# Kernel optimization log

Measured on AMD Instinct MI355X. Metric: run time of the kernel, lower is better.

The kernel has to match this reference:

```python
import jax, jax.numpy as jnp
import numpy as np

B, N, C = 2, 2048, 768
H = 12
HD = C // H  # 64
EPS = 1e-6


def setup_inputs() -> dict:
    key = jax.random.key(0)
    ks = jax.random.split(key, 6)
    x = jax.random.normal(ks[0], (B, N, C), dtype=jnp.float32)
    # Xavier-uniform-ish init for kernels
    lim_qkv = float(np.sqrt(6.0 / (C + 3 * C)))
    lim_proj = float(np.sqrt(6.0 / (C + C)))
    qkv_kernel = jax.random.uniform(ks[1], (C, 3 * C), minval=-lim_qkv, maxval=lim_qkv, dtype=jnp.float32)
    qkv_bias = jnp.zeros((3 * C,), dtype=jnp.float32)
    proj_kernel = jax.random.uniform(ks[2], (C, C), minval=-lim_proj, maxval=lim_proj, dtype=jnp.float32)
    proj_bias = jnp.zeros((C,), dtype=jnp.float32)
    q_norm_w = jnp.ones((HD,), dtype=jnp.float32)
    k_norm_w = jnp.ones((HD,), dtype=jnp.float32)
    # Standard RoPE tables: freqs over half the head dim, tiled to full head_dim
    half = HD // 2
    inv_freq = 1.0 / (10000.0 ** (jnp.arange(0, half, dtype=jnp.float32) / half))
    t = jnp.arange(N, dtype=jnp.float32)
    freqs = jnp.outer(t, inv_freq)               # (N, HD/2)
    emb = jnp.concatenate([freqs, freqs], axis=-1)  # (N, HD)
    rope_cos = jnp.cos(emb)
    rope_sin = jnp.sin(emb)
    return {"x": x, "rope_cos": rope_cos, "rope_sin": rope_sin,
            "qkv_kernel": qkv_kernel, "qkv_bias": qkv_bias,
            "proj_kernel": proj_kernel, "proj_bias": proj_bias,
            "q_norm_w": q_norm_w, "k_norm_w": k_norm_w}


def _rms_norm(x, w):
    var = jnp.mean(x * x, axis=-1, keepdims=True)
    return x * jax.lax.rsqrt(var + EPS) * w


def _rope(x, cos, sin):
    # x: (B, H, N, HD); cos/sin: (N, HD)
    half = x.shape[-1] // 2
    x1, x2 = x[..., :half], x[..., half:]
    rot = jnp.concatenate([-x2, x1], axis=-1)
    return x * cos + rot * sin


def reference(x, rope_cos, rope_sin, qkv_kernel, qkv_bias, proj_kernel, proj_bias, q_norm_w, k_norm_w):
    b, n, c = x.shape
    qkv = x @ qkv_kernel + qkv_bias                       # (B, N, 3C)
    qkv = qkv.reshape(b, n, 3, H, HD).transpose(2, 0, 3, 1, 4)  # (3, B, H, N, HD)
    q, k, v = qkv[0], qkv[1], qkv[2]
    q = _rope(_rms_norm(q, q_norm_w), rope_cos, rope_sin)
    k = _rope(_rms_norm(k, k_norm_w), rope_cos, rope_sin)
    scale = 1.0 / jnp.sqrt(jnp.float32(HD)).astype(x.dtype)
    attn = jnp.einsum('bhqd,bhkd->bhqk', q, k) * scale    # (B, H, N, N)
    attn = jax.nn.softmax(attn, axis=-1)
    out = jnp.einsum('bhqk,bhkd->bhqd', attn, v)          # (B, H, N, HD)
    out = out.swapaxes(1, 2).reshape(b, n, c)
    return out @ proj_kernel + proj_bias
```

## Files before the change

### kernel.cpp

```cpp
#include <hip/hip_runtime.h>
#include <math.h>

#define B_    2
#define N_    2048
#define C_    768
#define H_    12
#define HD_   64
#define NROWS (B_*N_)
#define QKVC  (3*C_)
#define EPSV  1e-6f
#define SCALE 0.125f
#define LOG2E 1.44269504088896f
#define SMAX  12.0f

typedef unsigned short u16;
typedef short bf16x8 __attribute__((ext_vector_type(8)));
typedef float f32x4  __attribute__((ext_vector_type(4)));

__device__ __forceinline__ float b2f(u16 u) {
    unsigned v = ((unsigned)u) << 16;
    return __builtin_bit_cast(float, v);
}
__device__ __forceinline__ u16 f2b(float f) {
    unsigned u = __builtin_bit_cast(unsigned, f);
    u += 0x7fffu + ((u >> 16) & 1u);
    return (u16)(u >> 16);
}
__device__ __forceinline__ unsigned pk2(float a, float b) {
#if __has_builtin(__builtin_amdgcn_cvt_pk_bf16_f32)
    auto r = __builtin_amdgcn_cvt_pk_bf16_f32(a, b);
    return __builtin_bit_cast(unsigned, r);
#else
    return (unsigned)f2b(a) | ((unsigned)f2b(b) << 16);
#endif
}
__device__ __forceinline__ float fexp2(float x) {
#if __has_builtin(__builtin_amdgcn_exp2f)
    return __builtin_amdgcn_exp2f(x);
#else
    return exp2f(x);
#endif
}
__device__ __forceinline__ void gload_lds16(const void* g, void* l) {
    __builtin_amdgcn_global_load_lds(
        (const __attribute__((address_space(1))) unsigned int*)g,
        (__attribute__((address_space(3))) unsigned int*)l, 16, 0, 0);
}

__global__ __launch_bounds__(256)
void cvt_bf16_kernel(const float* __restrict__ src, u16* __restrict__ dst) {
    const int i = (blockIdx.x * 256 + threadIdx.x) * 4;
    const float4 v = *(const float4*)(src + i);
    uint2 o = { pk2(v.x, v.y), pk2(v.z, v.w) };
    *(uint2*)(dst + i) = o;
}

__global__ __launch_bounds__(256)
void wtrans_kernel(const float* __restrict__ W, u16* __restrict__ Wt,
                   int K, int N) {
    __shared__ float T[64][65];
    const int k0 = blockIdx.y * 64, n0 = blockIdx.x * 64;
    const int t = threadIdx.x, r = t >> 6, c = t & 63;
#pragma unroll
    for (int p = 0; p < 16; ++p) {
        const int kl = p * 4 + r;
        T[kl][c] = W[(size_t)(k0 + kl) * N + n0 + c];
    }
    __syncthreads();
#pragma unroll
    for (int p = 0; p < 16; ++p) {
        const int nl = p * 4 + r;
        Wt[(size_t)(n0 + nl) * K + k0 + c] = f2b(T[c][nl]);
    }
}

template <bool BF16OUT>
__global__ __launch_bounds__(256)
void gemm_tn_kernel(const u16* __restrict__ A, const u16* __restrict__ Bt,
                    const float* __restrict__ bias, void* __restrict__ Cout,
                    int M, int N, int K) {
    __shared__ __attribute__((aligned(16))) u16 As[128 * 32];
    __shared__ __attribute__((aligned(16))) u16 Bs[128 * 32];
    const int tid = threadIdx.x;
    const int w = tid >> 6, l = tid & 63;
    const int lq = l & 15, quad = l >> 4;
    const int mbase = blockIdx.y * 128, nbase = blockIdx.x * 128;

    f32x4 acc[4][4];
    const f32x4 z4 = {0.f, 0.f, 0.f, 0.f};
#pragma unroll
    for (int mb = 0; mb < 4; ++mb)
#pragma unroll
        for (int nb = 0; nb < 4; ++nb) acc[mb][nb] = z4;

    const int srow = (l >> 2);
    const int sdc  = (l & 3) ^ ((l >> 2) & 3);

    for (int k0 = 0; k0 < K; k0 += 32) {
#pragma unroll
        for (int cc = 0; cc < 2; ++cc) {
            const int c = 2 * w + cc;
            const int row = 16 * c + srow;
            gload_lds16(A  + (size_t)(mbase + row) * K + k0 + sdc * 8, &As[c * 512]);
            gload_lds16(Bt + (size_t)(nbase + row) * K + k0 + sdc * 8, &Bs[c * 512]);
        }
        __syncthreads();

        bf16x8 af[4], bfr[4];
#pragma unroll
        for (int mb = 0; mb < 4; ++mb)
            af[mb] = *(const bf16x8*)
                &As[((w >> 1) * 64 + mb * 16 + lq) * 32 + ((quad ^ (lq & 3)) * 8)];
#pragma unroll
        for (int nb = 0; nb < 4; ++nb)
            bfr[nb] = *(const bf16x8*)
                &Bs[((w & 1) * 64 + nb * 16 + lq) * 32 + ((quad ^ (lq & 3)) * 8)];
#pragma unroll
        for (int mb = 0; mb < 4; ++mb)
#pragma unroll
            for (int nb = 0; nb < 4; ++nb)
                acc[mb][nb] = __builtin_amdgcn_mfma_f32_16x16x32_bf16(
                    af[mb], bfr[nb], acc[mb][nb], 0, 0, 0);
        __syncthreads();
    }

#pragma unroll
    for (int nb = 0; nb < 4; ++nb) {
        const int col = nbase + (w & 1) * 64 + nb * 16 + lq;
        const float bv = bias[col];
#pragma unroll
        for (int mb = 0; mb < 4; ++mb) {
#pragma unroll
            for (int r = 0; r < 4; ++r) {
                const int row = mbase + (w >> 1) * 64 + mb * 16 + quad * 4 + r;
                const float v = acc[mb][nb][r] + bv;
                if (BF16OUT) ((u16*)Cout)[(size_t)row * N + col] = f2b(v);
                else         ((float*)Cout)[(size_t)row * N + col] = v;
            }
        }
    }
}

__global__ __launch_bounds__(256)
void normrope_kernel(u16* __restrict__ qkv, u16* __restrict__ kpack,
                     const float* __restrict__ cosb,
                     const float* __restrict__ sinb,
                     const float* __restrict__ qw,
                     const float* __restrict__ kw) {
    const int item = blockIdx.x * 16 + (threadIdx.x >> 4);
    const int lq   = threadIdx.x & 15;
    const int h    = item % H_;
    const int row  = item / H_;
    const int n    = row & (N_ - 1);
    const int b    = row >> 11;
    const size_t base = (size_t)row * QKVC + h * HD_ + lq * 4;

    const ushort4 q4 = *(const ushort4*)&qkv[base];
    const ushort4 k4 = *(const ushort4*)&qkv[base + C_];
    float qf[4], kf[4];
    qf[0] = b2f(q4.x); qf[1] = b2f(q4.y); qf[2] = b2f(q4.z); qf[3] = b2f(q4.w);
    kf[0] = b2f(k4.x); kf[1] = b2f(k4.y); kf[2] = b2f(k4.z); kf[3] = b2f(k4.w);

    float q2 = qf[0]*qf[0] + qf[1]*qf[1] + qf[2]*qf[2] + qf[3]*qf[3];
    float k2 = kf[0]*kf[0] + kf[1]*kf[1] + kf[2]*kf[2] + kf[3]*kf[3];
#pragma unroll
    for (int off = 8; off >= 1; off >>= 1) {
        q2 += __shfl_xor(q2, off, 64);
        k2 += __shfl_xor(k2, off, 64);
    }
    const float rq = rsqrtf(q2 * (1.f / 64.f) + EPSV);
    const float rk = rsqrtf(k2 * (1.f / 64.f) + EPSV);

    const float4 qwv = *(const float4*)&qw[lq * 4];
    const float4 kwv = *(const float4*)&kw[lq * 4];
    const float4 cv  = *(const float4*)&cosb[n * HD_ + lq * 4];
    const float4 sv  = *(const float4*)&sinb[n * HD_ + lq * 4];

    float qn[4], kn[4];
    qn[0] = qf[0]*rq*qwv.x; qn[1] = qf[1]*rq*qwv.y;
    qn[2] = qf[2]*rq*qwv.z; qn[3] = qf[3]*rq*qwv.w;
    kn[0] = kf[0]*rk*kwv.x; kn[1] = kf[1]*rk*kwv.y;
    kn[2] = kf[2]*rk*kwv.z; kn[3] = kf[3]*rk*kwv.w;

    const float sgn = (lq < 8) ? -1.f : 1.f;
    float qo[4], ko[4];
    const float cc[4] = {cv.x, cv.y, cv.z, cv.w};
    const float ss[4] = {sv.x, sv.y, sv.z, sv.w};
#pragma unroll
    for (int j = 0; j < 4; ++j) {
        const float qp = __shfl_xor(qn[j], 8, 64);
        const float kp = __shfl_xor(kn[j], 8, 64);
        qo[j] = (qn[j] * cc[j] + sgn * qp * ss[j]) * (SCALE * LOG2E);
        ko[j] =  kn[j] * cc[j] + sgn * kp * ss[j];
    }
    uint2 qout = { pk2(qo[0], qo[1]), pk2(qo[2], qo[3]) };
    uint2 kout = { pk2(ko[0], ko[1]), pk2(ko[2], ko[3]) };
    *(uint2*)&qkv[base] = qout;

    const int kt = n >> 6, kr = n & 63;
    const int kb = kr >> 4, m = kr & 15;
    const int ks = lq >> 3, quad = (lq >> 1) & 3, jj = (lq & 1) * 4;
    const size_t off = ((size_t)(b * H_ + h) * 32 + kt) * 4096
                     + (size_t)((kb * 2 + ks) * 64 + quad * 16 + m) * 8 + jj;
    *(uint2*)&kpack[off] = kout;
}

__global__ __launch_bounds__(256)
void vpack_kernel(const u16* __restrict__ qkv, u16* __restrict__ vpack) {
    __shared__ u16 Tv[64][72];
    const int kt = blockIdx.x, bh = blockIdx.y;
    const int b = bh / H_, h = bh % H_;
    const int t = threadIdx.x;
    {
        const int r = t >> 2, seg = t & 3;
        const u16* src = &qkv[(size_t)(b * N_ + kt * 64 + r) * QKVC
                              + 2 * C_ + h * HD_ + seg * 16];
        const uint4 v0 = *(const uint4*)src;
        const uint4 v1 = *(const uint4*)(src + 8);
        *(uint4*)&Tv[r][seg * 16]     = v0;
        *(uint4*)&Tv[r][seg * 16 + 8] = v1;
    }
    __syncthreads();
    u16 tmp[16];
#pragma unroll
    for (int g2 = 0; g2 < 2; ++g2) {
        const int g = t * 2 + g2;
        const int mbks = g >> 6;
        const int l  = g & 63;
        const int mb = mbks >> 1, ks = mbks & 1;
        const int m  = l & 15,  quad = l >> 4;
#pragma unroll
        for (int j = 0; j < 8; ++j)
            tmp[g2 * 8 + j] = Tv[ks * 32 + quad * 8 + j][mb * 16 + m];
    }
    u16* dst = &vpack[((size_t)bh * 32 + kt) * 4096 + t * 16];
    *(uint4*)dst       = *(const uint4*)&tmp[0];
    *(uint4*)(dst + 8) = *(const uint4*)&tmp[8];
}

__global__ __launch_bounds__(128, 2)
void flash_mfma_kernel(const u16* __restrict__ qkv,
                       const u16* __restrict__ kpack,
                       const u16* __restrict__ vpack,
                       u16* __restrict__ attnb) {
    __shared__ __attribute__((aligned(16))) u16 Ps[2][64 * 64];
    __shared__ __attribute__((aligned(16))) float Oex[64 * 64];
    __shared__ float lex[64];

    const int tid = threadIdx.x;
    const int w = tid >> 6, l = tid & 63;
    const int lq = l & 15, quad = l >> 4;
    const int sw = lq & 7;

    const int lin  = blockIdx.x;
    const int slot = lin >> 3;
    const int bh   = (lin & 7) * 3 + (slot >> 5);
    const int qt   = slot & 31;
    const int b = bh / H_, h = bh % H_;
    const size_t qbase = (size_t)b * N_ * QKVC + h * HD_;
    const size_t tbase = (size_t)bh * 32 * 4096;

    bf16x8 qb[4][2];
#pragma unroll
    for (int nq = 0; nq < 4; ++nq)
#pragma unroll
        for (int ks = 0; ks < 2; ++ks)
            qb[nq][ks] = *(const bf16x8*)
                &qkv[qbase + (size_t)(qt * 64 + nq * 16 + lq) * QKVC
                     + ks * 32 + quad * 8];

    float lsum[4] = {0.f, 0.f, 0.f, 0.f};
    f32x4 oacc[4][4];
    const f32x4 z4 = {0.f, 0.f, 0.f, 0.f};
#pragma unroll
    for (int mb = 0; mb < 4; ++mb)
#pragma unroll
        for (int nq = 0; nq < 4; ++nq) oacc[mb][nq] = z4;

    bf16x8 ka[4][2];
#pragma unroll
    for (int kb = 0; kb < 4; ++kb)
#pragma unroll
        for (int ks = 0; ks < 2; ++ks)
            ka[kb][ks] = *(const bf16x8*)
                &kpack[tbase + (size_t)w * 4096 + ((kb * 2 + ks) * 64 + l) * 8];

    for (int kt2 = 0; kt2 < 16; ++kt2) {
        const int kt  = 2 * kt2 + w;
        const int ktn = (kt + 2) & 31;
        const size_t vb = tbase + (size_t)kt * 4096;
        const size_t kb_n = tbase + (size_t)ktn * 4096;

        bf16x8 va[4][2];
#pragma unroll
        for (int mb = 0; mb < 4; ++mb)
#pragma unroll
            for (int ks = 0; ks < 2; ++ks)
                va[mb][ks] = *(const bf16x8*)
                    &vpack[vb + ((mb * 2 + ks) * 64 + l) * 8];

#pragma unroll
        for (int kb = 0; kb < 4; ++kb) {
            f32x4 sacc[4];
#pragma unroll
            for (int nq = 0; nq < 4; ++nq) sacc[nq] = z4;
#pragma unroll
            for (int ks = 0; ks < 2; ++ks)
#pragma unroll
                for (int nq = 0; nq < 4; ++nq)
                    sacc[nq] = __builtin_amdgcn_mfma_f32_16x16x32_bf16(
                        ka[kb][ks], qb[nq][ks], sacc[nq], 0, 0, 0);
#pragma unroll
            for (int nq = 0; nq < 4; ++nq) {
                float p[4];
#pragma unroll
                for (int r = 0; r < 4; ++r) p[r] = fexp2(sacc[nq][r] - SMAX);
                lsum[nq] += (p[0] + p[1]) + (p[2] + p[3]);
                uint2 pkv = { pk2(p[0], p[1]), pk2(p[2], p[3]) };
                *(uint2*)&Ps[w][(nq * 16 + lq) * 64
                                + (((kb * 2 + (quad >> 1)) ^ sw) * 8)
                                + (quad & 1) * 4] = pkv;
            }
        }

#pragma unroll
        for (int kb = 0; kb < 4; ++kb)
#pragma unroll
            for (int ks = 0; ks < 2; ++ks)
                ka[kb][ks] = *(const bf16x8*)
                    &kpack[kb_n + ((kb * 2 + ks) * 64 + l) * 8];

        bf16x8 pb[2][4];
#pragma unroll
        for (int ks = 0; ks < 2; ++ks)
#pragma unroll
            for (int nq = 0; nq < 4; ++nq)
                pb[ks][nq] = *(const bf16x8*)
                    &Ps[w][(nq * 16 + lq) * 64 + (((ks * 4 + quad) ^ sw) * 8)];

#pragma unroll
        for (int mb = 0; mb < 4; ++mb)
#pragma unroll
            for (int ks = 0; ks < 2; ++ks)
#pragma unroll
                for (int nq = 0; nq < 4; ++nq)
                    oacc[mb][nq] = __builtin_amdgcn_mfma_f32_16x16x32_bf16(
                        va[mb][ks], pb[ks][nq], oacc[mb][nq], 0, 0, 0);
    }

#pragma unroll
    for (int nq = 0; nq < 4; ++nq) {
        lsum[nq] += __shfl_xor(lsum[nq], 16, 64);
        lsum[nq] += __shfl_xor(lsum[nq], 32, 64);
    }

    if (w == 1) {
#pragma unroll
        for (int nq = 0; nq < 4; ++nq) {
#pragma unroll
            for (int mb = 0; mb < 4; ++mb) {
                const int chunk = (mb * 4 + quad) ^ lq;
                *(float4*)&Oex[(nq * 16 + lq) * 64 + chunk * 4] =
                    *(float4*)&oacc[mb][nq];
            }
            if (quad == 0) lex[nq * 16 + lq] = lsum[nq];
        }
    }
    __syncthreads();
    if (w == 0) {
#pragma unroll
        for (int nq = 0; nq < 4; ++nq) {
            const int qrow = nq * 16 + lq;
            const float inv = 1.f / (lsum[nq] + lex[qrow]);
#pragma unroll
            for (int mb = 0; mb < 4; ++mb) {
                const int chunk = (mb * 4 + quad) ^ lq;
                const float4 oe = *(const float4*)&Oex[qrow * 64 + chunk * 4];
                const float o0 = (oacc[mb][nq][0] + oe.x) * inv;
                const float o1 = (oacc[mb][nq][1] + oe.y) * inv;
                const float o2 = (oacc[mb][nq][2] + oe.z) * inv;
                const float o3 = (oacc[mb][nq][3] + oe.w) * inv;
                uint2 ov = { pk2(o0, o1), pk2(o2, o3) };
                *(uint2*)&Ps[0][qrow * 64
                                + (((mb * 2 + (quad >> 1)) ^ sw) * 8)
                                + (quad & 1) * 4] = ov;
            }
        }
#pragma unroll
        for (int pass = 0; pass < 8; ++pass) {
            const int ql = pass * 8 + (l >> 3);
            const int c  = l & 7;
            const bf16x8 v = *(const bf16x8*)&Ps[0][ql * 64 + ((c ^ (ql & 7)) * 8)];
            const int query = qt * 64 + ql;
            *(bf16x8*)&attnb[(size_t)(b * N_ + query) * C_ + h * HD_ + c * 8] = v;
        }
    }
}

extern "C" void kernel_launch(void* const* d_in, const int* in_sizes, int n_in,
                              void* d_out, int out_size, void* d_ws, size_t ws_size,
                              hipStream_t stream) {
    const float* x        = (const float*)d_in[0];
    const float* rope_cos = (const float*)d_in[1];
    const float* rope_sin = (const float*)d_in[2];
    const float* qkv_w    = (const float*)d_in[3];
    const float* qkv_b    = (const float*)d_in[4];
    const float* proj_w   = (const float*)d_in[5];
    const float* proj_b   = (const float*)d_in[6];
    const float* q_nw     = (const float*)d_in[7];
    const float* k_nw     = (const float*)d_in[8];
    float* out = (float*)d_out;

    u16* xb    = (u16*)d_ws;
    u16* qwt   = xb    + (size_t)NROWS * C_;
    u16* pwt   = qwt   + (size_t)QKVC * C_;
    u16* qkvb  = pwt   + (size_t)C_ * C_;
    u16* vpackb= qkvb  + (size_t)NROWS * QKVC;
    u16* attnb = vpackb+ (size_t)B_ * H_ * 32 * 4096;
    u16* kpackb= xb;

    cvt_bf16_kernel<<<dim3(NROWS * C_ / 1024), 256, 0, stream>>>(x, xb);
    wtrans_kernel<<<dim3(QKVC / 64, C_ / 64), 256, 0, stream>>>(qkv_w, qwt, C_, QKVC);
    wtrans_kernel<<<dim3(C_ / 64, C_ / 64), 256, 0, stream>>>(proj_w, pwt, C_, C_);

    gemm_tn_kernel<true><<<dim3(QKVC / 128, NROWS / 128), 256, 0, stream>>>(
        xb, qwt, qkv_b, qkvb, NROWS, QKVC, C_);

    normrope_kernel<<<dim3(NROWS * H_ / 16), 256, 0, stream>>>(
        qkvb, kpackb, rope_cos, rope_sin, q_nw, k_nw);

    vpack_kernel<<<dim3(32, B_ * H_), 256, 0, stream>>>(qkvb, vpackb);

    flash_mfma_kernel<<<dim3(32 * B_ * H_ / 4 * 4), 128, 0, stream>>>(
        qkvb, kpackb, vpackb, attnb);

    gemm_tn_kernel<false><<<dim3(C_ / 128, NROWS / 128), 256, 0, stream>>>(
        attnb, pwt, proj_b, out, NROWS, C_, C_);
}
```

Measured before the change: 196.6 us.

## Split attention KV loop across four waves and merge normrope with vpack

The flash attention block grows from 2 to 4 waves. Each wave handles every fourth KV tile, and the partial outputs are reduced serially through shared memory, after which all waves share the final normalization and store. The norm/RoPE and V-pack kernels are fused into a single launch that picks its role by block index, which removes one launch. The design adds more shared memory (Ps is doubled) and serialized reduction barriers, and it may lower occupancy with launch bounds of 256,3. It also appears to index Ps[w] for w up to 3, which matches the doubled buffer.

```diff
diff --git a/kernel.cpp b/kernel.cpp
--- a/kernel.cpp
+++ b/kernel.cpp
@@ -142,108 +142,109 @@
 }
 
 __global__ __launch_bounds__(256)
-void normrope_kernel(u16* __restrict__ qkv, u16* __restrict__ kpack,
-                     const float* __restrict__ cosb,
-                     const float* __restrict__ sinb,
-                     const float* __restrict__ qw,
-                     const float* __restrict__ kw) {
-    const int item = blockIdx.x * 16 + (threadIdx.x >> 4);
-    const int lq   = threadIdx.x & 15;
-    const int h    = item % H_;
-    const int row  = item / H_;
-    const int n    = row & (N_ - 1);
-    const int b    = row >> 11;
-    const size_t base = (size_t)row * QKVC + h * HD_ + lq * 4;
-
-    const ushort4 q4 = *(const ushort4*)&qkv[base];
-    const ushort4 k4 = *(const ushort4*)&qkv[base + C_];
-    float qf[4], kf[4];
-    qf[0] = b2f(q4.x); qf[1] = b2f(q4.y); qf[2] = b2f(q4.z); qf[3] = b2f(q4.w);
-    kf[0] = b2f(k4.x); kf[1] = b2f(k4.y); kf[2] = b2f(k4.z); kf[3] = b2f(k4.w);
-
-    float q2 = qf[0]*qf[0] + qf[1]*qf[1] + qf[2]*qf[2] + qf[3]*qf[3];
-    float k2 = kf[0]*kf[0] + kf[1]*kf[1] + kf[2]*kf[2] + kf[3]*kf[3];
-#pragma unroll
-    for (int off = 8; off >= 1; off >>= 1) {
-        q2 += __shfl_xor(q2, off, 64);
-        k2 += __shfl_xor(k2, off, 64);
-    }
-    const float rq = rsqrtf(q2 * (1.f / 64.f) + EPSV);
-    const float rk = rsqrtf(k2 * (1.f / 64.f) + EPSV);
-
-    const float4 qwv = *(const float4*)&qw[lq * 4];
-    const float4 kwv = *(const float4*)&kw[lq * 4];
-    const float4 cv  = *(const float4*)&cosb[n * HD_ + lq * 4];
-    const float4 sv  = *(const float4*)&sinb[n * HD_ + lq * 4];
-
-    float qn[4], kn[4];
-    qn[0] = qf[0]*rq*qwv.x; qn[1] = qf[1]*rq*qwv.y;
-    qn[2] = qf[2]*rq*qwv.z; qn[3] = qf[3]*rq*qwv.w;
-    kn[0] = kf[0]*rk*kwv.x; kn[1] = kf[1]*rk*kwv.y;
-    kn[2] = kf[2]*rk*kwv.z; kn[3] = kf[3]*rk*kwv.w;
-
-    const float sgn = (lq < 8) ? -1.f : 1.f;
-    float qo[4], ko[4];
-    const float cc[4] = {cv.x, cv.y, cv.z, cv.w};
-    const float ss[4] = {sv.x, sv.y, sv.z, sv.w};
-#pragma unroll
-    for (int j = 0; j < 4; ++j) {
-        const float qp = __shfl_xor(qn[j], 8, 64);
-        const float kp = __shfl_xor(kn[j], 8, 64);
-        qo[j] = (qn[j] * cc[j] + sgn * qp * ss[j]) * (SCALE * LOG2E);
-        ko[j] =  kn[j] * cc[j] + sgn * kp * ss[j];
-    }
-    uint2 qout = { pk2(qo[0], qo[1]), pk2(qo[2], qo[3]) };
-    uint2 kout = { pk2(ko[0], ko[1]), pk2(ko[2], ko[3]) };
-    *(uint2*)&qkv[base] = qout;
-
-    const int kt = n >> 6, kr = n & 63;
-    const int kb = kr >> 4, m = kr & 15;
-    const int ks = lq >> 3, quad = (lq >> 1) & 3, jj = (lq & 1) * 4;
-    const size_t off = ((size_t)(b * H_ + h) * 32 + kt) * 4096
-                     + (size_t)((kb * 2 + ks) * 64 + quad * 16 + m) * 8 + jj;
-    *(uint2*)&kpack[off] = kout;
-}
-
-__global__ __launch_bounds__(256)
-void vpack_kernel(const u16* __restrict__ qkv, u16* __restrict__ vpack) {
-    __shared__ u16 Tv[64][72];
-    const int kt = blockIdx.x, bh = blockIdx.y;
-    const int b = bh / H_, h = bh % H_;
-    const int t = threadIdx.x;
-    {
-        const int r = t >> 2, seg = t & 3;
-        const u16* src = &qkv[(size_t)(b * N_ + kt * 64 + r) * QKVC
-                              + 2 * C_ + h * HD_ + seg * 16];
-        const uint4 v0 = *(const uint4*)src;
-        const uint4 v1 = *(const uint4*)(src + 8);
-        *(uint4*)&Tv[r][seg * 16]     = v0;
-        *(uint4*)&Tv[r][seg * 16 + 8] = v1;
-    }
-    __syncthreads();
-    u16 tmp[16];
-#pragma unroll
-    for (int g2 = 0; g2 < 2; ++g2) {
-        const int g = t * 2 + g2;
-        const int mbks = g >> 6;
-        const int l  = g & 63;
-        const int mb = mbks >> 1, ks = mbks & 1;
-        const int m  = l & 15,  quad = l >> 4;
-#pragma unroll
-        for (int j = 0; j < 8; ++j)
-            tmp[g2 * 8 + j] = Tv[ks * 32 + quad * 8 + j][mb * 16 + m];
-    }
-    u16* dst = &vpack[((size_t)bh * 32 + kt) * 4096 + t * 16];
-    *(uint4*)dst       = *(const uint4*)&tmp[0];
-    *(uint4*)(dst + 8) = *(const uint4*)&tmp[8];
-}
-
-__global__ __launch_bounds__(128, 2)
+void normrope_vpack_kernel(u16* __restrict__ qkv, u16* __restrict__ kpack,
+                           u16* __restrict__ vpack,
+                           const float* __restrict__ cosb,
+                           const float* __restrict__ sinb,
+                           const float* __restrict__ qw,
+                           const float* __restrict__ kw) {
+    if (blockIdx.x < 3072) {
+        const int item = blockIdx.x * 16 + (threadIdx.x >> 4);
+        const int lq   = threadIdx.x & 15;
+        const int h    = item % H_;
+        const int row  = item / H_;
+        const int n    = row & (N_ - 1);
+        const int b    = row >> 11;
+        const size_t base = (size_t)row * QKVC + h * HD_ + lq * 4;
+
+        const ushort4 q4 = *(const ushort4*)&qkv[base];
+        const ushort4 k4 = *(const ushort4*)&qkv[base + C_];
+        float qf[4], kf[4];
+        qf[0] = b2f(q4.x); qf[1] = b2f(q4.y); qf[2] = b2f(q4.z); qf[3] = b2f(q4.w);
+        kf[0] = b2f(k4.x); kf[1] = b2f(k4.y); kf[2] = b2f(k4.z); kf[3] = b2f(k4.w);
+
+        float q2 = qf[0]*qf[0] + qf[1]*qf[1] + qf[2]*qf[2] + qf[3]*qf[3];
+        float k2 = kf[0]*kf[0] + kf[1]*kf[1] + kf[2]*kf[2] + kf[3]*kf[3];
+#pragma unroll
+        for (int off = 8; off >= 1; off >>= 1) {
+            q2 += __shfl_xor(q2, off, 64);
+            k2 += __shfl_xor(k2, off, 64);
+        }
+        const float rq = rsqrtf(q2 * (1.f / 64.f) + EPSV);
+        const float rk = rsqrtf(k2 * (1.f / 64.f) + EPSV);
+
+        const float4 qwv = *(const float4*)&qw[lq * 4];
+        const float4 kwv = *(const float4*)&kw[lq * 4];
+        const float4 cv  = *(const float4*)&cosb[n * HD_ + lq * 4];
+        const float4 sv  = *(const float4*)&sinb[n * HD_ + lq * 4];
+
+        float qn[4], kn[4];
+        qn[0] = qf[0]*rq*qwv.x; qn[1] = qf[1]*rq*qwv.y;
+        qn[2] = qf[2]*rq*qwv.z; qn[3] = qf[3]*rq*qwv.w;
+        kn[0] = kf[0]*rk*kwv.x; kn[1] = kf[1]*rk*kwv.y;
+        kn[2] = kf[2]*rk*kwv.z; kn[3] = kf[3]*rk*kwv.w;
+
+        const float sgn = (lq < 8) ? -1.f : 1.f;
+        float qo[4], ko[4];
+        const float cc[4] = {cv.x, cv.y, cv.z, cv.w};
+        const float ss[4] = {sv.x, sv.y, sv.z, sv.w};
+#pragma unroll
+        for (int j = 0; j < 4; ++j) {
+            const float qp = __shfl_xor(qn[j], 8, 64);
+            const float kp = __shfl_xor(kn[j], 8, 64);
+            qo[j] = (qn[j] * cc[j] + sgn * qp * ss[j]) * (SCALE * LOG2E);
+            ko[j] =  kn[j] * cc[j] + sgn * kp * ss[j];
+        }
+        uint2 qout = { pk2(qo[0], qo[1]), pk2(qo[2], qo[3]) };
+        uint2 kout = { pk2(ko[0], ko[1]), pk2(ko[2], ko[3]) };
+        *(uint2*)&qkv[base] = qout;
+
+        const int kt = n >> 6, kr = n & 63;
+        const int kb = kr >> 4, m = kr & 15;
+        const int ks = lq >> 3, quad = (lq >> 1) & 3, jj = (lq & 1) * 4;
+        const size_t off = ((size_t)(b * H_ + h) * 32 + kt) * 4096
+                         + (size_t)((kb * 2 + ks) * 64 + quad * 16 + m) * 8 + jj;
+        *(uint2*)&kpack[off] = kout;
+    } else {
+        __shared__ u16 Tv[64][72];
+        const int idx = blockIdx.x - 3072;
+        const int kt = idx & 31, bh = idx >> 5;
+        const int b = bh / H_, h = bh % H_;
+        const int t = threadIdx.x;
+        {
+            const int r = t >> 2, seg = t & 3;
+            const u16* src = &qkv[(size_t)(b * N_ + kt * 64 + r) * QKVC
+                                  + 2 * C_ + h * HD_ + seg * 16];
+            const uint4 v0 = *(const uint4*)src;
+            const uint4 v1 = *(const uint4*)(src + 8);
+            *(uint4*)&Tv[r][seg * 16]     = v0;
+            *(uint4*)&Tv[r][seg * 16 + 8] = v1;
+        }
+        __syncthreads();
+        u16 tmp[16];
+#pragma unroll
+        for (int g2 = 0; g2 < 2; ++g2) {
+            const int g = t * 2 + g2;
+            const int mbks = g >> 6;
+            const int l  = g & 63;
+            const int mb = mbks >> 1, ks = mbks & 1;
+            const int m  = l & 15,  quad = l >> 4;
+#pragma unroll
+            for (int j = 0; j < 8; ++j)
+                tmp[g2 * 8 + j] = Tv[ks * 32 + quad * 8 + j][mb * 16 + m];
+        }
+        u16* dst = &vpack[((size_t)bh * 32 + kt) * 4096 + t * 16];
+        *(uint4*)dst       = *(const uint4*)&tmp[0];
+        *(uint4*)(dst + 8) = *(const uint4*)&tmp[8];
+    }
+}
+
+__global__ __launch_bounds__(256, 3)
 void flash_mfma_kernel(const u16* __restrict__ qkv,
                        const u16* __restrict__ kpack,
                        const u16* __restrict__ vpack,
                        u16* __restrict__ attnb) {
-    __shared__ __attribute__((aligned(16))) u16 Ps[2][64 * 64];
+    __shared__ __attribute__((aligned(16))) u16 Ps[4][64 * 64];
     __shared__ __attribute__((aligned(16))) float Oex[64 * 64];
     __shared__ float lex[64];
 
@@ -285,10 +286,10 @@
             ka[kb][ks] = *(const bf16x8*)
                 &kpack[tbase + (size_t)w * 4096 + ((kb * 2 + ks) * 64 + l) * 8];
 
-    for (int kt2 = 0; kt2 < 16; ++kt2) {
-        const int kt  = 2 * kt2 + w;
-        const int ktn = (kt + 2) & 31;
-        const size_t vb = tbase + (size_t)kt * 4096;
+    for (int kt2 = 0; kt2 < 8; ++kt2) {
+        const int kt  = 4 * kt2 + w;
+        const int ktn = (kt + 4) & 31;
+        const size_t vb   = tbase + (size_t)kt * 4096;
         const size_t kb_n = tbase + (size_t)ktn * 4096;
 
         bf16x8 va[4][2];
@@ -354,46 +355,50 @@
         lsum[nq] += __shfl_xor(lsum[nq], 32, 64);
     }
 
-    if (w == 1) {
+    if (w == 0) {
 #pragma unroll
         for (int nq = 0; nq < 4; ++nq) {
 #pragma unroll
             for (int mb = 0; mb < 4; ++mb) {
-                const int chunk = (mb * 4 + quad) ^ lq;
-                *(float4*)&Oex[(nq * 16 + lq) * 64 + chunk * 4] =
-                    *(float4*)&oacc[mb][nq];
+                const int chunkS = (mb * 4 + quad) ^ lq;
+                float4 v;
+                v.x = oacc[mb][nq][0]; v.y = oacc[mb][nq][1];
+                v.z = oacc[mb][nq][2]; v.w = oacc[mb][nq][3];
+                *(float4*)&Oex[(nq * 16 + lq) * 64 + chunkS * 4] = v;
             }
             if (quad == 0) lex[nq * 16 + lq] = lsum[nq];
         }
     }
     __syncthreads();
-    if (w == 0) {
-#pragma unroll
-        for (int nq = 0; nq < 4; ++nq) {
-            const int qrow = nq * 16 + lq;
-            const float inv = 1.f / (lsum[nq] + lex[qrow]);
-#pragma unroll
-            for (int mb = 0; mb < 4; ++mb) {
-                const int chunk = (mb * 4 + quad) ^ lq;
-                const float4 oe = *(const float4*)&Oex[qrow * 64 + chunk * 4];
-                const float o0 = (oacc[mb][nq][0] + oe.x) * inv;
-                const float o1 = (oacc[mb][nq][1] + oe.y) * inv;
-                const float o2 = (oacc[mb][nq][2] + oe.z) * inv;
-                const float o3 = (oacc[mb][nq][3] + oe.w) * inv;
-                uint2 ov = { pk2(o0, o1), pk2(o2, o3) };
-                *(uint2*)&Ps[0][qrow * 64
-                                + (((mb * 2 + (quad >> 1)) ^ sw) * 8)
-                                + (quad & 1) * 4] = ov;
+#pragma unroll
+    for (int ww = 1; ww < 4; ++ww) {
+        if (w == ww) {
+#pragma unroll
+            for (int nq = 0; nq < 4; ++nq) {
+#pragma unroll
+                for (int mb = 0; mb < 4; ++mb) {
+                    const int chunkS = (mb * 4 + quad) ^ lq;
+                    float4* p = (float4*)&Oex[(nq * 16 + lq) * 64 + chunkS * 4];
+                    float4 v = *p;
+                    v.x += oacc[mb][nq][0]; v.y += oacc[mb][nq][1];
+                    v.z += oacc[mb][nq][2]; v.w += oacc[mb][nq][3];
+                    *p = v;
+                }
+                if (quad == 0) lex[nq * 16 + lq] += lsum[nq];
             }
         }
-#pragma unroll
-        for (int pass = 0; pass < 8; ++pass) {
-            const int ql = pass * 8 + (l >> 3);
-            const int c  = l & 7;
-            const bf16x8 v = *(const bf16x8*)&Ps[0][ql * 64 + ((c ^ (ql & 7)) * 8)];
-            const int query = qt * 64 + ql;
-            *(bf16x8*)&attnb[(size_t)(b * N_ + query) * C_ + h * HD_ + c * 8] = v;
-        }
+        __syncthreads();
+    }
+
+#pragma unroll
+    for (int pass = 0; pass < 4; ++pass) {
+        const int qloc = w * 16 + pass * 4 + quad;
+        const int key  = qloc & 15;
+        const float inv = 1.f / lex[qloc];
+        const float4 ov = *(const float4*)&Oex[qloc * 64 + ((lq ^ key) * 4)];
+        uint2 o2 = { pk2(ov.x * inv, ov.y * inv), pk2(ov.z * inv, ov.w * inv) };
+        const int query = qt * 64 + qloc;
+        *(uint2*)&attnb[(size_t)(b * N_ + query) * C_ + h * HD_ + lq * 4] = o2;
     }
 }
 
@@ -426,12 +431,10 @@
     gemm_tn_kernel<true><<<dim3(QKVC / 128, NROWS / 128), 256, 0, stream>>>(
         xb, qwt, qkv_b, qkvb, NROWS, QKVC, C_);
 
-    normrope_kernel<<<dim3(NROWS * H_ / 16), 256, 0, stream>>>(
-        qkvb, kpackb, rope_cos, rope_sin, q_nw, k_nw);
-
-    vpack_kernel<<<dim3(32, B_ * H_), 256, 0, stream>>>(qkvb, vpackb);
-
-    flash_mfma_kernel<<<dim3(32 * B_ * H_ / 4 * 4), 128, 0, stream>>>(
+    normrope_vpack_kernel<<<dim3(3072 + 768), 256, 0, stream>>>(
+        qkvb, kpackb, vpackb, rope_cos, rope_sin, q_nw, k_nw);
+
+    flash_mfma_kernel<<<dim3(768), 256, 0, stream>>>(
         qkvb, kpackb, vpackb, attnb);
 
     gemm_tn_kernel<false><<<dim3(C_ / 128, NROWS / 128), 256, 0, stream>>>(
```

Result: slower. 253.2 us (+28.8%).
